# Optimization experiments

Hardware: AMD Instinct MI355X
Metric: run time of the kernel (lower is better)

The kernel has to match this reference:

```python
import jax, jax.numpy as jnp
import numpy as np

EPS = 1e-7
GAMMA = 2.0
ALPHA = 0.5


def focal_loss(y_true, y_pred):
    # elementwise focal loss on sigmoid probs; y_true is 0/1 int
    pos = -ALPHA * (1.0 - y_pred) ** GAMMA * jnp.log(y_pred + EPS)
    neg = -(1.0 - ALPHA) * y_pred ** GAMMA * jnp.log(1.0 - y_pred + EPS)
    return jnp.where(y_true == 1, pos, neg)


def setup_inputs() -> dict:
    B, N, D, L = 4, 1024, 768, 16
    key = jax.random.key(0)
    ks = jax.random.split(key, 8)
    x = jax.random.normal(ks[0], (B, N, D), dtype=jnp.float32)
    start = jax.random.randint(ks[1], (B, L, N), 0, 2, dtype=jnp.int32)
    end = jax.random.randint(ks[2], (B, L, N), 0, 2, dtype=jnp.int32)
    span = jax.random.randint(ks[3], (B, L, N, N), 0, 2, dtype=jnp.int32)
    val = jax.random.randint(ks[4], (B, L, N, N), 0, 2, dtype=jnp.int32)
    seqlen = jax.random.randint(ks[5], (B,), N // 2, N + 1, dtype=jnp.int32).at[0].set(N)
    w_se = jax.random.normal(ks[6], (D, 2 * L), dtype=jnp.float32) * 0.02
    b_se = jnp.zeros((2 * L,), dtype=jnp.float32)
    w_sp = jax.random.normal(ks[7], (2 * D, L), dtype=jnp.float32) * 0.02
    b_sp = jnp.zeros((L,), dtype=jnp.float32)
    return {"x": x, "start": start, "end": end, "span": span, "val": val,
            "seqlen": seqlen, "w_se": w_se, "b_se": b_se, "w_sp": w_sp, "b_sp": b_sp}


def reference(x, start, end, span, val, seqlen, w_se, b_se, w_sp, b_sp):
    B, N, D = x.shape
    L2 = w_se.shape[1]
    # start/end head: Dense(2L, sigmoid) then transpose -> [B, 2L, N]
    startend_output = jnp.transpose(jax.nn.sigmoid(x @ w_se + b_se), (0, 2, 1))
    seqmask = (jnp.arange(N) < seqlen[:, None]).astype(jnp.int32)[:, None, :]  # [B,1,N]
    startend_predict = (startend_output > 0.5).astype(jnp.int32) * seqmask
    start_predict, end_predict = jnp.split(startend_predict, 2, axis=1)  # each [B,L,N]
    startend = jnp.concatenate([start, end], axis=1)  # [B,2L,N]
    maskf = jnp.broadcast_to(seqmask.astype(jnp.float32), (B, L2, N))
    startend_loss = jnp.sum(focal_loss(startend, startend_output) * maskf) / jnp.sum(maskf)

    # span head: biaffine decomposition of Dense over tiled concat([startx, endx])
    # concat(x_i, x_j) @ W + b == x_i @ W[:D] + x_j @ W[D:] + b  (identical math)
    sx = x @ w_sp[:D]  # [B,N,L]
    ex = x @ w_sp[D:]  # [B,N,L]
    logits = sx[:, :, None, :] + ex[:, None, :, :] + b_sp  # [B,N,N,L]
    span_output = jnp.transpose(jax.nn.sigmoid(logits), (0, 3, 1, 2))  # [B,L,N,N]

    triu = jnp.triu(jnp.ones((N, N), dtype=jnp.int32))  # j >= i (right-upper incl. diag)
    span_predict = ((span_output > 0.5).astype(jnp.int32)
                    * start_predict[:, :, :, None]
                    * end_predict[:, :, None, :]
                    * triu)

    valf = val.astype(jnp.float32)
    accuracy = (span_predict == span).astype(jnp.float32) * valf
    valsum = jnp.sum(valf)
    accuracysum = jnp.sum(accuracy)
    span_loss = jnp.sum(focal_loss(span, span_output) * valf) / (valsum + EPS)
    loss = 0.15 * startend_loss + 0.7 * span_loss

    tp = jnp.sum(((span == 1) & (span_predict == 1)).astype(jnp.float32))
    tn = jnp.sum(((span == 1) & (span_predict != 1)).astype(jnp.float32))
    fp = jnp.sum(((span == 0) & (span_predict == 1)).astype(jnp.float32))
    return (span_predict, start_predict, end_predict, tp, tn, fp, loss, accuracysum, valsum)
```

## Files before the change

kernel.cpp:

```cpp
#include <hip/hip_runtime.h>
#include <math.h>

#define B_ 4
#define N_ 1024
#define D_ 768
#define L_ 16
#define DC_ 192
#define EPSF 1e-7f

typedef unsigned long long ull;

__global__ __launch_bounds__(256) void head_kernel(
    const float* __restrict__ x, const int* __restrict__ start, const int* __restrict__ end,
    const int* __restrict__ seqlen,
    const float* __restrict__ w_se, const float* __restrict__ b_se,
    const float* __restrict__ w_sp, const float* __restrict__ b_sp,
    float* __restrict__ out_start, float* __restrict__ out_end,
    float* __restrict__ sx_t, float* __restrict__ ex_t,
    int* __restrict__ spi, int* __restrict__ epi,
    float* __restrict__ part_se)
{
  __shared__ float xt[8][D_];
  __shared__ float xw[DC_][64];
  __shared__ float smf[4];
  int bid = blockIdx.x;
  int b  = bid >> 7;
  int n0 = (bid & 127) << 3;
  int tid = threadIdx.x;

  {
    float4* xt4 = (float4*)xt;
    const float4* x4 = (const float4*)(x + (size_t)(b * N_ + n0) * D_);
    for (int idx = tid; idx < 8 * D_ / 4; idx += 256) xt4[idx] = x4[idx];
  }

  int col  = tid >> 2;
  int part = tid & 3;
  float acc[8] = {0.f,0.f,0.f,0.f,0.f,0.f,0.f,0.f};

  for (int c = 0; c < D_ / DC_; ++c) {
    int d0 = c * DC_;
    __syncthreads();
    for (int idx = tid; idx < DC_ * 8; idx += 256) {
      int dd = idx >> 3, cc = idx & 7;
      ((float4*)&xw[dd][0])[cc] = ((const float4*)(w_se + (size_t)(d0 + dd) * 32))[cc];
    }
    for (int idx = tid; idx < DC_ * 4; idx += 256) {
      int dd = idx >> 2, cc = idx & 3;
      ((float4*)&xw[dd][32])[cc] = ((const float4*)(w_sp + (size_t)(d0 + dd) * 16))[cc];
      ((float4*)&xw[dd][48])[cc] = ((const float4*)(w_sp + (size_t)(D_ + d0 + dd) * 16))[cc];
    }
    __syncthreads();
    for (int d = part; d < DC_; d += 4) {
      float wv = xw[d][col];
#pragma unroll
      for (int r = 0; r < 8; ++r) acc[r] += xt[r][d0 + d] * wv;
    }
  }

#pragma unroll
  for (int r = 0; r < 8; ++r) {
    acc[r] += __shfl_xor(acc[r], 1, 64);
    acc[r] += __shfl_xor(acc[r], 2, 64);
  }

  float fl = 0.f;
  if (part == 0) {
    int sl = seqlen[b];
    if (col < 32) {
      float bse = b_se[col];
#pragma unroll
      for (int r = 0; r < 8; ++r) {
        int n = n0 + r;
        int mask = (n < sl) ? 1 : 0;
        float z = acc[r] + bse;
        float p = 1.f / (1.f + expf(-z));
        int pred = (z > 0.f && mask) ? 1 : 0;
        int y = (col < L_) ? start[((b * L_ + col) << 10) | n]
                           : end[((b * L_ + (col - L_)) << 10) | n];
        float f = (y == 1) ? (-0.5f * (1.f - p) * (1.f - p) * logf(p + EPSF))
                           : (-0.5f * p * p * logf(1.f - p + EPSF));
        fl += mask ? f : 0.f;
        int o = ((b * L_ + (col & (L_ - 1))) << 10) | n;
        if (col < L_) { out_start[o] = (float)pred; spi[o] = pred; }
        else          { out_end[o]   = (float)pred; epi[o] = pred; }
      }
    } else if (col < 48) {
      int l = col - 32;
      float bb = b_sp[l];
#pragma unroll
      for (int r = 0; r < 8; ++r)
        sx_t[((b * L_ + l) << 10) | (n0 + r)] = acc[r] + bb;
    } else {
      int l = col - 48;
#pragma unroll
      for (int r = 0; r < 8; ++r)
        ex_t[((b * L_ + l) << 10) | (n0 + r)] = acc[r];
    }
  }
  for (int o = 32; o > 0; o >>= 1) fl += __shfl_down(fl, o, 64);
  int wid = tid >> 6, lane = tid & 63;
  if (lane == 0) smf[wid] = fl;
  __syncthreads();
  if (tid == 0) part_se[bid] = smf[0] + smf[1] + smf[2] + smf[3];
}

__global__ __launch_bounds__(256) void span_kernel(
    const int* __restrict__ span, const int* __restrict__ val,
    const float* __restrict__ sx_t, const float* __restrict__ ex_t,
    const int* __restrict__ spi, const int* __restrict__ epi,
    float* __restrict__ out_span,
    float* __restrict__ part)
{
  const float L2E = 1.44269504f;
  const float LN2 = 0.69314718f;

  int bid = blockIdx.x;
  int bl  = bid >> 7;
  int i0  = (bid & 127) << 3;
  int tid = threadIdx.x;

  float4 e4  = ((const float4*)(ex_t + ((size_t)bl << 10)))[tid];
  int4   ep4 = ((const int4*  )(epi  + ((size_t)bl << 10)))[tid];

  float s_r[8]; int sp_r[8];
#pragma unroll
  for (int r = 0; r < 8; ++r) {
    s_r[r]  = sx_t[(bl << 10) | (i0 + r)];
    sp_r[r] = spi [(bl << 10) | (i0 + r)] ? 1 : 0;
  }

  size_t base = (((size_t)bl << 10) | (size_t)i0) << 10;
  const int4* yrow = (const int4*)(span + base);
  const int4* vrow = (const int4*)(val  + base);
  float4*     orow = (float4*)(out_span + base);

  int4 ya[8], va[8];
#pragma unroll
  for (int r = 0; r < 8; ++r) ya[r] = yrow[r * 256 + tid];
#pragma unroll
  for (int r = 0; r < 8; ++r) va[r] = vrow[r * 256 + tid];

  int j0 = tid << 2;
  float lsum = 0.f;
  int a1 = 0, a2 = 0, a3 = 0;

#pragma unroll
  for (int r = 0; r < 8; ++r) {
    int i = i0 + r;
    float s = s_r[r];
    int sp_i = sp_r[r];
    float4 o4;
#pragma unroll
    for (int k = 0; k < 4; ++k) {
      int j   = j0 + k;
      int y   = ((const int*)&ya[r])[k];
      int vv  = ((const int*)&va[r])[k];
      float e = ((const float*)&e4)[k];
      int ep  = ((const int*)&ep4)[k];

      float z  = s + e;
      float em = __builtin_amdgcn_exp2f(z * -L2E);
      float dn = 1.f + em;
      float pr = __builtin_amdgcn_rcpf(dn);
      float U  = __builtin_amdgcn_logf(dn);
      float omp = em * pr;
      bool  yp  = (y != 0);
      float tsel = yp ? omp : pr;
      float Lv   = fmaf(U, LN2, yp ? 0.f : z);
      float fv   = tsel * tsel * Lv;
      lsum += vv ? fv : 0.f;

      int gate = (ep & sp_i) & ((j >= i) ? 1 : 0);
      int predi = (z > 0.f) ? gate : 0;
      ((float*)&o4)[k] = (float)predi;

      a1 += y + (predi << 16);
      a2 += (y & predi) + (vv << 16);
      a3 += (predi == y) ? vv : 0;
    }
    orow[r * 256 + tid] = o4;
  }

  for (int o = 32; o > 0; o >>= 1) {
    lsum += __shfl_down(lsum, o, 64);
    a1   += __shfl_down(a1,   o, 64);
    a2   += __shfl_down(a2,   o, 64);
    a3   += __shfl_down(a3,   o, 64);
  }
  __shared__ float smf[4];
  __shared__ int   smi[3][4];
  int wid = tid >> 6, lane = tid & 63;
  if (lane == 0) { smf[wid] = lsum; smi[0][wid] = a1; smi[1][wid] = a2; smi[2][wid] = a3; }
  __syncthreads();
  if (tid == 0) {
    float ls = smf[0] + smf[1] + smf[2] + smf[3];
    int r1 = smi[0][0] + smi[0][1] + smi[0][2] + smi[0][3];
    int r2 = smi[1][0] + smi[1][1] + smi[1][2] + smi[1][3];
    int r3 = smi[2][0] + smi[2][1] + smi[2][2] + smi[2][3];
    int S_y = r1 & 0xffff, S_p = r1 >> 16;
    int S_yp = r2 & 0xffff, S_v = r2 >> 16;
    float* p = part + (size_t)bid * 8;
    p[0] = 0.5f * ls;
    p[1] = (float)S_v;
    p[2] = (float)r3;
    p[3] = (float)S_yp;
    p[4] = (float)(S_y - S_yp);
    p[5] = (float)(S_p - S_yp);
  }
}

__global__ __launch_bounds__(256) void reduce_kernel(
    const float* __restrict__ part,
    const float* __restrict__ part_se,
    double* __restrict__ acc)
{
  int g = blockIdx.x;
  float s[6] = {0.f, 0.f, 0.f, 0.f, 0.f, 0.f};
  for (int r = threadIdx.x; r < 128; r += 256) {
    const float* p = part + (size_t)(g * 128 + r) * 8;
    s[0] += p[0]; s[1] += p[1]; s[2] += p[2];
    s[3] += p[3]; s[4] += p[4]; s[5] += p[5];
  }
  float se = (threadIdx.x < 8) ? part_se[g * 8 + threadIdx.x] : 0.f;

  for (int o = 32; o > 0; o >>= 1) {
    for (int q = 0; q < 6; ++q) s[q] += __shfl_down(s[q], o, 64);
    se += __shfl_down(se, o, 64);
  }
  __shared__ float smf[7][4];
  int wid = threadIdx.x >> 6, lane = threadIdx.x & 63;
  if (lane == 0) { for (int q = 0; q < 6; ++q) smf[q][wid] = s[q]; smf[6][wid] = se; }
  __syncthreads();
  if (threadIdx.x == 0) {
    atomicAdd(&acc[1], (double)(smf[0][0] + smf[0][1] + smf[0][2] + smf[0][3]));
    atomicAdd(&acc[2], (double)(smf[1][0] + smf[1][1] + smf[1][2] + smf[1][3]));
    atomicAdd(&acc[3], (double)(smf[2][0] + smf[2][1] + smf[2][2] + smf[2][3]));
    atomicAdd(&acc[4], (double)(smf[3][0] + smf[3][1] + smf[3][2] + smf[3][3]));
    atomicAdd(&acc[5], (double)(smf[4][0] + smf[4][1] + smf[4][2] + smf[4][3]));
    atomicAdd(&acc[6], (double)(smf[5][0] + smf[5][1] + smf[5][2] + smf[5][3]));
    atomicAdd(&acc[0], (double)(smf[6][0] + smf[6][1] + smf[6][2] + smf[6][3]));
  }
}

__global__ void finalize_kernel(const double* __restrict__ acc,
                                const int* __restrict__ seqlen,
                                float* __restrict__ out_scal)
{
  if (threadIdx.x == 0) {
    double masks = 2.0 * L_ * (double)(seqlen[0] + seqlen[1] + seqlen[2] + seqlen[3]);
    double sel  = acc[0] / masks;
    double spl  = acc[1] / (acc[2] + 1e-7);
    double loss = 0.15 * sel + 0.7 * spl;
    out_scal[0] = (float)acc[4];
    out_scal[1] = (float)acc[5];
    out_scal[2] = (float)acc[6];
    out_scal[3] = (float)loss;
    out_scal[4] = (float)acc[3];
    out_scal[5] = (float)acc[2];
  }
}

extern "C" void kernel_launch(void* const* d_in, const int* in_sizes, int n_in,
                              void* d_out, int out_size, void* d_ws, size_t ws_size,
                              hipStream_t stream) {
  const float* x      = (const float*)d_in[0];
  const int*   start  = (const int*)  d_in[1];
  const int*   end    = (const int*)  d_in[2];
  const int*   span   = (const int*)  d_in[3];
  const int*   val    = (const int*)  d_in[4];
  const int*   seqlen = (const int*)  d_in[5];
  const float* w_se   = (const float*)d_in[6];
  const float* b_se   = (const float*)d_in[7];
  const float* w_sp   = (const float*)d_in[8];
  const float* b_sp   = (const float*)d_in[9];

  float* out = (float*)d_out;
  const size_t span_elems = (size_t)B_ * L_ * N_ * N_;
  const size_t se_elems   = (size_t)B_ * L_ * N_;
  float* out_span  = out;
  float* out_start = out + span_elems;
  float* out_end   = out_start + se_elems;
  float* out_scal  = out_end + se_elems;

  char* ws = (char*)d_ws;
  double* acc     = (double*)ws;
  float*  sx_t    = (float*)(ws + 64);
  float*  ex_t    = (float*)(ws + 64 + 262144);
  int*    spi     = (int*)  (ws + 64 + 2 * 262144);
  int*    epi     = (int*)  (ws + 64 + 3 * 262144);
  float*  part    = (float*)(ws + 64 + 4 * 262144);
  float*  part_se = (float*)(ws + 64 + 4 * 262144 + 262144);

  (void)hipMemsetAsync(acc, 0, 64, stream);

  head_kernel<<<512, 256, 0, stream>>>(
      x, start, end, seqlen, w_se, b_se, w_sp, b_sp,
      out_start, out_end, sx_t, ex_t, spi, epi, part_se);

  span_kernel<<<8192, 256, 0, stream>>>(
      span, val, sx_t, ex_t, spi, epi, out_span, part);

  reduce_kernel<<<64, 256, 0, stream>>>(part, part_se, acc);

  finalize_kernel<<<1, 64, 0, stream>>>(acc, seqlen, out_scal);
}
```

Baseline: 205.7 us.

## Swizzle span block order, stream loads per row, merge reduce and finalize

The span kernel now remaps block indices so that consecutive workgroups, likely spread across XCDs, touch widely separated rows. Span and val loads move inside the per-row loop, trading full upfront prefetch for lower register pressure. The atomic-based reduce, finalize kernel and memset are replaced by a single 1024-thread block that reduces all partials and writes the scalars, removing two launches and a memset. The single-block reduction may be slower to read 8192 partials, and the in-loop loads may expose more memory latency.

```diff
diff --git a/kernel.cpp b/kernel.cpp
--- a/kernel.cpp
+++ b/kernel.cpp
@@ -115,7 +115,8 @@
   const float L2E = 1.44269504f;
   const float LN2 = 0.69314718f;
 
-  int bid = blockIdx.x;
+  int obid = blockIdx.x;
+  int bid  = ((obid & 7) << 10) + (obid >> 3);
   int bl  = bid >> 7;
   int i0  = (bid & 127) << 3;
   int tid = threadIdx.x;
@@ -135,18 +136,14 @@
   const int4* vrow = (const int4*)(val  + base);
   float4*     orow = (float4*)(out_span + base);
 
-  int4 ya[8], va[8];
-#pragma unroll
-  for (int r = 0; r < 8; ++r) ya[r] = yrow[r * 256 + tid];
-#pragma unroll
-  for (int r = 0; r < 8; ++r) va[r] = vrow[r * 256 + tid];
-
   int j0 = tid << 2;
   float lsum = 0.f;
   int a1 = 0, a2 = 0, a3 = 0;
 
 #pragma unroll
   for (int r = 0; r < 8; ++r) {
+    int4 y4 = yrow[r * 256 + tid];
+    int4 v4 = vrow[r * 256 + tid];
     int i = i0 + r;
     float s = s_r[r];
     int sp_i = sp_r[r];
@@ -154,8 +151,8 @@
 #pragma unroll
     for (int k = 0; k < 4; ++k) {
       int j   = j0 + k;
-      int y   = ((const int*)&ya[r])[k];
-      int vv  = ((const int*)&va[r])[k];
+      int y   = ((const int*)&y4)[k];
+      int vv  = ((const int*)&v4)[k];
       float e = ((const float*)&e4)[k];
       int ep  = ((const int*)&ep4)[k];
 
@@ -210,54 +207,46 @@
   }
 }
 
-__global__ __launch_bounds__(256) void reduce_kernel(
+__global__ __launch_bounds__(1024) void reduce_final_kernel(
     const float* __restrict__ part,
     const float* __restrict__ part_se,
-    double* __restrict__ acc)
+    const int* __restrict__ seqlen,
+    float* __restrict__ out_scal)
 {
-  int g = blockIdx.x;
+  int tid = threadIdx.x;
   float s[6] = {0.f, 0.f, 0.f, 0.f, 0.f, 0.f};
-  for (int r = threadIdx.x; r < 128; r += 256) {
-    const float* p = part + (size_t)(g * 128 + r) * 8;
+  for (int r = tid; r < 8192; r += 1024) {
+    const float* p = part + (size_t)r * 8;
     s[0] += p[0]; s[1] += p[1]; s[2] += p[2];
     s[3] += p[3]; s[4] += p[4]; s[5] += p[5];
   }
-  float se = (threadIdx.x < 8) ? part_se[g * 8 + threadIdx.x] : 0.f;
+  float se = (tid < 512) ? part_se[tid] : 0.f;
 
   for (int o = 32; o > 0; o >>= 1) {
     for (int q = 0; q < 6; ++q) s[q] += __shfl_down(s[q], o, 64);
     se += __shfl_down(se, o, 64);
   }
-  __shared__ float smf[7][4];
-  int wid = threadIdx.x >> 6, lane = threadIdx.x & 63;
-  if (lane == 0) { for (int q = 0; q < 6; ++q) smf[q][wid] = s[q]; smf[6][wid] = se; }
+  __shared__ double sm[7][16];
+  int wid = tid >> 6, lane = tid & 63;
+  if (lane == 0) {
+    for (int q = 0; q < 6; ++q) sm[q][wid] = (double)s[q];
+    sm[6][wid] = (double)se;
+  }
   __syncthreads();
-  if (threadIdx.x == 0) {
-    atomicAdd(&acc[1], (double)(smf[0][0] + smf[0][1] + smf[0][2] + smf[0][3]));
-    atomicAdd(&acc[2], (double)(smf[1][0] + smf[1][1] + smf[1][2] + smf[1][3]));
-    atomicAdd(&acc[3], (double)(smf[2][0] + smf[2][1] + smf[2][2] + smf[2][3]));
-    atomicAdd(&acc[4], (double)(smf[3][0] + smf[3][1] + smf[3][2] + smf[3][3]));
-    atomicAdd(&acc[5], (double)(smf[4][0] + smf[4][1] + smf[4][2] + smf[4][3]));
-    atomicAdd(&acc[6], (double)(smf[5][0] + smf[5][1] + smf[5][2] + smf[5][3]));
-    atomicAdd(&acc[0], (double)(smf[6][0] + smf[6][1] + smf[6][2] + smf[6][3]));
-  }
-}
-
-__global__ void finalize_kernel(const double* __restrict__ acc,
-                                const int* __restrict__ seqlen,
-                                float* __restrict__ out_scal)
-{
-  if (threadIdx.x == 0) {
+  if (tid == 0) {
+    double t[7] = {0,0,0,0,0,0,0};
+    for (int w = 0; w < 16; ++w)
+      for (int q = 0; q < 7; ++q) t[q] += sm[q][w];
     double masks = 2.0 * L_ * (double)(seqlen[0] + seqlen[1] + seqlen[2] + seqlen[3]);
-    double sel  = acc[0] / masks;
-    double spl  = acc[1] / (acc[2] + 1e-7);
+    double sel  = t[6] / masks;
+    double spl  = t[0] / (t[1] + 1e-7);
     double loss = 0.15 * sel + 0.7 * spl;
-    out_scal[0] = (float)acc[4];
-    out_scal[1] = (float)acc[5];
-    out_scal[2] = (float)acc[6];
+    out_scal[0] = (float)t[3];
+    out_scal[1] = (float)t[4];
+    out_scal[2] = (float)t[5];
     out_scal[3] = (float)loss;
-    out_scal[4] = (float)acc[3];
-    out_scal[5] = (float)acc[2];
+    out_scal[4] = (float)t[2];
+    out_scal[5] = (float)t[1];
   }
 }
 
@@ -284,7 +273,6 @@
   float* out_scal  = out_end + se_elems;
 
   char* ws = (char*)d_ws;
-  double* acc     = (double*)ws;
   float*  sx_t    = (float*)(ws + 64);
   float*  ex_t    = (float*)(ws + 64 + 262144);
   int*    spi     = (int*)  (ws + 64 + 2 * 262144);
@@ -292,8 +280,6 @@
   float*  part    = (float*)(ws + 64 + 4 * 262144);
   float*  part_se = (float*)(ws + 64 + 4 * 262144 + 262144);
 
-  (void)hipMemsetAsync(acc, 0, 64, stream);
-
   head_kernel<<<512, 256, 0, stream>>>(
       x, start, end, seqlen, w_se, b_se, w_sp, b_sp,
       out_start, out_end, sx_t, ex_t, spi, epi, part_se);
@@ -301,7 +287,5 @@
   span_kernel<<<8192, 256, 0, stream>>>(
       span, val, sx_t, ex_t, spi, epi, out_span, part);
 
-  reduce_kernel<<<64, 256, 0, stream>>>(part, part_se, acc);
-
-  finalize_kernel<<<1, 64, 0, stream>>>(acc, seqlen, out_scal);
-}
+  reduce_final_kernel<<<1, 1024, 0, stream>>>(part, part_se, seqlen, out_scal);
+}
```

After: 218.8 us. 1.06x slower.
